# Kernel optimization log

Hardware: AMD Instinct MI355X
Metric: run time of the kernel (lower is better)

## Reference

```python
import jax, jax.numpy as jnp
import numpy as np

DIM = 2048
NUM_HEADS = 16
HEAD_DIM = DIM // NUM_HEADS
SCALE = 1.0 / float(np.sqrt(HEAD_DIM))


def setup_inputs() -> dict:
    key = jax.random.key(0)
    ks = jax.random.split(key, 7)
    B, L = 2, 2048
    x = jax.random.normal(ks[0], (B, L, DIM), dtype=jnp.float32)
    s = 1.0 / np.sqrt(DIM)
    # nn.Linear stores weight as [out, in]; y = x @ W.T + b
    Wq = jax.random.uniform(ks[1], (DIM, DIM), jnp.float32, -s, s)
    bq = jax.random.uniform(ks[2], (DIM,), jnp.float32, -s, s)
    Wk = jax.random.uniform(ks[3], (DIM, DIM), jnp.float32, -s, s)
    bk = jax.random.uniform(ks[4], (DIM,), jnp.float32, -s, s)
    Wv = jax.random.uniform(ks[5], (DIM, DIM), jnp.float32, -s, s)
    bv = jax.random.uniform(ks[6], (DIM,), jnp.float32, -s, s)
    return {"x": x, "Wq": Wq, "bq": bq, "Wk": Wk, "bk": bk, "Wv": Wv, "bv": bv}


def _attn(x, Wq, bq, Wk, bk, Wv, bv):
    B, L, D = x.shape
    H, Hd = NUM_HEADS, HEAD_DIM
    # projections: x @ W.T + b, then split heads -> [B, H, L, Hd]
    q = (x @ Wq.T + bq).reshape(B, L, H, Hd).transpose(0, 2, 1, 3)
    k = (x @ Wk.T + bk).reshape(B, L, H, Hd).transpose(0, 2, 1, 3)
    v = (x @ Wv.T + bv).reshape(B, L, H, Hd).transpose(0, 2, 1, 3)
    scores = jnp.einsum("bhqd,bhkd->bhqk", q, k) * SCALE  # [B,H,L,L]
    attn = jax.nn.softmax(scores, axis=-1)
    out = jnp.einsum("bhqk,bhkd->bhqd", attn, v)
    return out.transpose(0, 2, 1, 3).reshape(B, L, D)


def reference(x, Wq, bq, Wk, bk, Wv, bv):
    return _attn(x, Wq, bq, Wk, bk, Wv, bv)
```

## Files before the change

### kernel.cpp

```cpp
#include <hip/hip_runtime.h>
#include <stdint.h>

typedef unsigned short u16;
typedef __attribute__((ext_vector_type(8))) short short8;
typedef __attribute__((ext_vector_type(16))) float f32x16;

#define ATTN_SCALE 0.08838834764831845f

__device__ __forceinline__ u16 f2bf(float f) {
  union { float f; uint32_t u; } a; a.f = f;
  return (u16)((a.u + 0x7fffu + ((a.u >> 16) & 1u)) >> 16);
}

__device__ __forceinline__ void async16(const u16* g, u16* lds) {
  __builtin_amdgcn_global_load_lds(
      (const __attribute__((address_space(1))) void*)g,
      (__attribute__((address_space(3))) void*)lds, 16, 0, 0);
}

__global__ void cvt_kernel(const float* __restrict__ src, u16* __restrict__ dst, int n8) {
  int i = blockIdx.x * 256 + threadIdx.x;
  if (i >= n8) return;
  const float4* s4 = (const float4*)src;
  float4 a = s4[2 * i], c = s4[2 * i + 1];
  union { u16 h[8]; uint4 v; } o;
  o.h[0] = f2bf(a.x); o.h[1] = f2bf(a.y); o.h[2] = f2bf(a.z); o.h[3] = f2bf(a.w);
  o.h[4] = f2bf(c.x); o.h[5] = f2bf(c.y); o.h[6] = f2bf(c.z); o.h[7] = f2bf(c.w);
  ((uint4*)dst)[i] = o.v;
}

__global__ void cvtw_kernel(const float* __restrict__ w0, const float* __restrict__ w1,
                            const float* __restrict__ w2, u16* __restrict__ dst) {
  int z = blockIdx.y;
  const float* src = (z == 0) ? w0 : (z == 1) ? w1 : w2;
  int i = blockIdx.x * 256 + threadIdx.x;
  const float4* s4 = (const float4*)src;
  float4 a = s4[2 * i], c = s4[2 * i + 1];
  union { u16 h[8]; uint4 v; } o;
  o.h[0] = f2bf(a.x); o.h[1] = f2bf(a.y); o.h[2] = f2bf(a.z); o.h[3] = f2bf(a.w);
  o.h[4] = f2bf(c.x); o.h[5] = f2bf(c.y); o.h[6] = f2bf(c.z); o.h[7] = f2bf(c.w);
  ((uint4*)(dst + (size_t)z * 4194304))[i] = o.v;
}

__global__ __launch_bounds__(512, 2) void qkv_gemm(
    const u16* __restrict__ xb, const u16* __restrict__ Wb,
    const float* __restrict__ bq, const float* __restrict__ bk, const float* __restrict__ bv,
    u16* __restrict__ qkv) {
  extern __shared__ __align__(16) u16 smem[];
  u16* As = smem;
  u16* Bs = smem + 32768;
  const int z = blockIdx.z;
  const int n0 = blockIdx.x * 256, m0 = blockIdx.y * 256;
  const u16* Bw = Wb + (size_t)z * 4194304u;
  const float* bias = (z == 0) ? bq : (z == 1) ? bk : bv;
  u16* dst = qkv + (size_t)z * 8388608u;
  const int t = threadIdx.x;
  const int wave = t >> 6, lane = t & 63;
  const int wm = wave >> 2, wn = wave & 3, l31 = lane & 31, h = lane >> 5;

  int soff[2], goff[2];
#pragma unroll
  for (int p = 0; p < 2; ++p) {
    const int s = p * 512 + t;
    const int R = s >> 4, j = s & 15, u = j ^ (R & 15);
    const int m = 4 * R + (u >> 2), c = u & 3;
    soff[p] = s * 8;
    goff[p] = m * 2048 + c * 8;
  }
  const int q4 = (l31 & 3) * 4;
  int fr16A[4], fR15A[4], fr16B[2], fR15B[2];
#pragma unroll
  for (int am = 0; am < 4; ++am) {
    const int mA = wm * 128 + am * 32 + l31;
    fr16A[am] = (mA >> 2) * 16; fR15A[am] = (mA >> 2) & 15;
  }
#pragma unroll
  for (int bn = 0; bn < 2; ++bn) {
    const int mB = wn * 64 + bn * 32 + l31;
    fr16B[bn] = (mB >> 2) * 16; fR15B[bn] = (mB >> 2) & 15;
  }

  f32x16 acc[4][2];
#pragma unroll
  for (int am = 0; am < 4; ++am)
#pragma unroll
    for (int bn = 0; bn < 2; ++bn)
#pragma unroll
      for (int r = 0; r < 16; ++r) acc[am][bn][r] = 0.f;

  const u16* Abase = xb + (size_t)m0 * 2048;
  const u16* Bbase = Bw + (size_t)n0 * 2048;

#pragma unroll
  for (int r = 0; r < 3; ++r) {
    const int k0 = r * 32;
#pragma unroll
    for (int p = 0; p < 2; ++p) async16(Abase + goff[p] + k0, &As[r * 8192 + soff[p]]);
#pragma unroll
    for (int p = 0; p < 2; ++p) async16(Bbase + goff[p] + k0, &Bs[r * 8192 + soff[p]]);
  }

#pragma unroll 1
  for (int kt = 0; kt < 64; ++kt) {
    if (kt <= 61)      asm volatile("s_waitcnt vmcnt(8)" ::: "memory");
    else if (kt == 62) asm volatile("s_waitcnt vmcnt(4)" ::: "memory");
    else               asm volatile("s_waitcnt vmcnt(0)" ::: "memory");
    __builtin_amdgcn_s_barrier();
    __builtin_amdgcn_sched_barrier(0);

    if (kt + 3 < 64) {
      const int k0 = (kt + 3) * 32, bn_ = (kt + 3) & 3;
#pragma unroll
      for (int p = 0; p < 2; ++p) async16(Abase + goff[p] + k0, &As[bn_ * 8192 + soff[p]]);
#pragma unroll
      for (int p = 0; p < 2; ++p) async16(Bbase + goff[p] + k0, &Bs[bn_ * 8192 + soff[p]]);
    }

    const u16* aL = As + (kt & 3) * 8192;
    const u16* bL = Bs + (kt & 3) * 8192;
#pragma unroll
    for (int kk = 0; kk < 2; ++kk) {
      const int c = kk * 2 + h;
      short8 af[4], bf[2];
#pragma unroll
      for (int am = 0; am < 4; ++am)
        af[am] = *(const short8*)&aL[(fr16A[am] + ((q4 + c) ^ fR15A[am])) * 8];
#pragma unroll
      for (int bn = 0; bn < 2; ++bn)
        bf[bn] = *(const short8*)&bL[(fr16B[bn] + ((q4 + c) ^ fR15B[bn])) * 8];
      __builtin_amdgcn_s_setprio(1);
#pragma unroll
      for (int am = 0; am < 4; ++am)
#pragma unroll
        for (int bn = 0; bn < 2; ++bn)
          acc[am][bn] = __builtin_amdgcn_mfma_f32_32x32x16_bf16(af[am], bf[bn], acc[am][bn], 0, 0, 0);
      __builtin_amdgcn_s_setprio(0);
    }
  }

#pragma unroll
  for (int bn = 0; bn < 2; ++bn) {
    const int col = n0 + wn * 64 + bn * 32 + l31;
    const float bb_ = bias[col];
    const int hh = col >> 7, hd = col & 127;
#pragma unroll
    for (int am = 0; am < 4; ++am) {
#pragma unroll
      for (int g = 0; g < 4; ++g) {
        const int lbase = m0 + wm * 128 + am * 32 + 8 * g + 4 * h;
        const int bb = lbase >> 11, l0 = lbase & 2047;
        if (z == 2) {
          union { u16 q[4]; uint2 d; } pk;
#pragma unroll
          for (int rr = 0; rr < 4; ++rr) pk.q[rr] = f2bf(acc[am][bn][4 * g + rr] + bb_);
          *(uint2*)&dst[((size_t)(bb * 16 + hh) * 128 + hd) * 2048 + l0] = pk.d;
        } else {
#pragma unroll
          for (int rr = 0; rr < 4; ++rr)
            dst[((size_t)(bb * 16 + hh) * 2048 + (l0 + rr)) * 128 + hd] =
                f2bf(acc[am][bn][4 * g + rr] + bb_);
        }
      }
    }
  }
}

__global__ __launch_bounds__(256, 2) void attn_kernel(
    const u16* __restrict__ Qg,
    const u16* __restrict__ Kg,
    const u16* __restrict__ Vtg,
    float* __restrict__ out) {
  __shared__ __align__(16) u16 Ks[2][64 * 128];
  __shared__ __align__(16) u16 Vs[2][128 * 64];
  const int bh = blockIdx.y, q0 = blockIdx.x * 128;
  const int t = threadIdx.x, wave = t >> 6, lane = t & 63;
  const int l31 = lane & 31, h = lane >> 5;
  const u16* Qp = Qg + (size_t)bh * 262144;
  const u16* Kp = Kg + (size_t)bh * 262144;
  const u16* Vp = Vtg + (size_t)bh * 262144;
  const int b = bh >> 4, hd = bh & 15;
  const int qrow = q0 + wave * 32 + l31;

  short8 qf[8];
#pragma unroll
  for (int s = 0; s < 8; ++s)
    qf[s] = *(const short8*)&Qp[(size_t)qrow * 128 + s * 16 + h * 8];

  int kOff[4], kSlot[4], vOff[4], vSlot[4];
#pragma unroll
  for (int p = 0; p < 4; ++p) {
    const int s = p * 256 + wave * 64 + lane;
    const int rk = s >> 4, gk = (s & 15) ^ (rk & 15);
    kSlot[p] = s * 8; kOff[p] = rk * 128 + gk * 8;
    const int rv = s >> 3, gv = (s & 7) ^ (rv & 7);
    vSlot[p] = s * 8; vOff[p] = rv * 2048 + gv * 8;
  }

  f32x16 oac[4];
#pragma unroll
  for (int dt = 0; dt < 4; ++dt)
#pragma unroll
    for (int r = 0; r < 16; ++r) oac[dt][r] = 0.f;
  float den = 0.f;

#pragma unroll
  for (int p = 0; p < 4; ++p) async16(Kp + kOff[p], &Ks[0][kSlot[p]]);
#pragma unroll
  for (int p = 0; p < 4; ++p) async16(Vp + vOff[p], &Vs[0][vSlot[p]]);

#pragma unroll 1
  for (int kt = 0; kt < 32; ++kt) {
    __syncthreads();
    const int cur = kt & 1;
    if (kt + 1 < 32) {
      const int k1 = (kt + 1) * 64;
#pragma unroll
      for (int p = 0; p < 4; ++p)
        async16(Kp + (size_t)k1 * 128 + kOff[p], &Ks[cur ^ 1][kSlot[p]]);
#pragma unroll
      for (int p = 0; p < 4; ++p)
        async16(Vp + (size_t)k1 + vOff[p], &Vs[cur ^ 1][vSlot[p]]);
    }

#pragma unroll
    for (int T = 0; T < 2; ++T) {
      const int krow = T * 32 + l31;
      f32x16 sc;
#pragma unroll
      for (int r = 0; r < 16; ++r) sc[r] = 0.f;
#pragma unroll
      for (int s = 0; s < 8; ++s) {
        const short8 kf = *(const short8*)&Ks[cur][(krow * 16 + ((2 * s + h) ^ (krow & 15))) * 8];
        sc = __builtin_amdgcn_mfma_f32_32x32x16_bf16(kf, qf[s], sc, 0, 0, 0);
      }
      uint32_t pp[8];
#pragma unroll
      for (int i = 0; i < 8; ++i) {
        const float e0 = __expf(fminf(sc[2 * i] * ATTN_SCALE, 80.f));
        const float e1 = __expf(fminf(sc[2 * i + 1] * ATTN_SCALE, 80.f));
        den += e0 + e1;
        union { float f; uint32_t u; } u0, u1; u0.f = e0; u1.f = e1;
        pp[i] = ((u1.u + 0x8000u) & 0xffff0000u) | ((u0.u + 0x8000u) >> 16);
      }
      uint32_t x[8];
#pragma unroll
      for (int i = 0; i < 8; ++i) x[i] = __shfl_xor(pp[i], 32, 64);
#pragma unroll
      for (int ks = 0; ks < 2; ++ks) {
        const int o0 = ks * 4;
        union { uint32_t u[4]; short8 s8; } bfp;
        bfp.u[0] = h ? x[o0 + 2] : pp[o0 + 0];
        bfp.u[1] = h ? x[o0 + 3] : pp[o0 + 1];
        bfp.u[2] = h ? pp[o0 + 2] : x[o0 + 0];
        bfp.u[3] = h ? pp[o0 + 3] : x[o0 + 1];
        const int gk = T * 4 + ks * 2 + h;
#pragma unroll
        for (int dt = 0; dt < 4; ++dt) {
          const int vrow = dt * 32 + l31;
          const short8 vf = *(const short8*)&Vs[cur][(vrow * 8 + (gk ^ (vrow & 7))) * 8];
          oac[dt] = __builtin_amdgcn_mfma_f32_32x32x16_bf16(vf, bfp.s8, oac[dt], 0, 0, 0);
        }
      }
    }
  }

  den += __shfl_xor(den, 32, 64);
  const float inv = 1.f / den;
#pragma unroll
  for (int dt = 0; dt < 4; ++dt) {
#pragma unroll
    for (int g4 = 0; g4 < 4; ++g4) {
      float4 o;
      o.x = oac[dt][4 * g4 + 0] * inv;
      o.y = oac[dt][4 * g4 + 1] * inv;
      o.z = oac[dt][4 * g4 + 2] * inv;
      o.w = oac[dt][4 * g4 + 3] * inv;
      const int d = dt * 32 + g4 * 8 + h * 4;
      *(float4*)&out[((size_t)(b * 2048 + qrow)) * 2048 + hd * 128 + d] = o;
    }
  }
}

extern "C" void kernel_launch(void* const* d_in, const int* in_sizes, int n_in,
                              void* d_out, int out_size, void* d_ws, size_t ws_size,
                              hipStream_t stream) {
  const float* x  = (const float*)d_in[0];
  const float* Wq = (const float*)d_in[1];
  const float* bq = (const float*)d_in[2];
  const float* Wk = (const float*)d_in[3];
  const float* bk = (const float*)d_in[4];
  const float* Wv = (const float*)d_in[5];
  const float* bv = (const float*)d_in[6];
  float* out = (float*)d_out;
  if (ws_size < 92274688u) return;

  u16* xb  = (u16*)d_ws;
  u16* Wb  = xb + 8388608;
  u16* qkv = Wb + 12582912;

  cvt_kernel<<<4096, 256, 0, stream>>>(x, xb, 1048576);
  cvtw_kernel<<<dim3(2048, 3), 256, 0, stream>>>(Wq, Wk, Wv, Wb);
  qkv_gemm<<<dim3(8, 16, 3), 512, 131072, stream>>>(xb, Wb, bq, bk, bv, qkv);
  attn_kernel<<<dim3(16, 32), 256, 0, stream>>>(qkv, qkv + 8388608, qkv + 16777216, out);
}
```

Before: 355.3 us.

## Restructure projection GEMM mainloop into interleaved four-phase ping-pong schedule

Rewrites the K-loop of the QKV projection GEMM to process two 32-wide K chunks per iteration in four phases. Each phase interleaves LDS fragment reads, async global-to-LDS prefetch of either A or B for the next step, and the MFMA burst, with barriers and vmcnt waits placed between phases. Prefetch depth drops from three chunks ahead to a two-chunk lookahead. The aim is to spread memory issue across MFMA work and overlap loads with compute more evenly, at the cost of more barriers per K step and a shorter prefetch distance.

```diff
diff --git a/kernel.cpp b/kernel.cpp
--- a/kernel.cpp
+++ b/kernel.cpp
@@ -92,42 +92,46 @@
   const u16* Bbase = Bw + (size_t)n0 * 2048;
 
 #pragma unroll
-  for (int r = 0; r < 3; ++r) {
-    const int k0 = r * 32;
-#pragma unroll
-    for (int p = 0; p < 2; ++p) async16(Abase + goff[p] + k0, &As[r * 8192 + soff[p]]);
-#pragma unroll
-    for (int p = 0; p < 2; ++p) async16(Bbase + goff[p] + k0, &Bs[r * 8192 + soff[p]]);
-  }
+  for (int ch = 0; ch < 2; ++ch) {
+    const int k0 = ch * 32;
+#pragma unroll
+    for (int p = 0; p < 2; ++p) async16(Abase + goff[p] + k0, &As[ch * 8192 + soff[p]]);
+#pragma unroll
+    for (int p = 0; p < 2; ++p) async16(Bbase + goff[p] + k0, &Bs[ch * 8192 + soff[p]]);
+  }
+  asm volatile("s_waitcnt vmcnt(4)" ::: "memory");
+  __builtin_amdgcn_s_barrier();
 
 #pragma unroll 1
-  for (int kt = 0; kt < 64; ++kt) {
-    if (kt <= 61)      asm volatile("s_waitcnt vmcnt(8)" ::: "memory");
-    else if (kt == 62) asm volatile("s_waitcnt vmcnt(4)" ::: "memory");
-    else               asm volatile("s_waitcnt vmcnt(0)" ::: "memory");
-    __builtin_amdgcn_s_barrier();
-    __builtin_amdgcn_sched_barrier(0);
-
-    if (kt + 3 < 64) {
-      const int k0 = (kt + 3) * 32, bn_ = (kt + 3) & 3;
-#pragma unroll
-      for (int p = 0; p < 2; ++p) async16(Abase + goff[p] + k0, &As[bn_ * 8192 + soff[p]]);
-#pragma unroll
-      for (int p = 0; p < 2; ++p) async16(Bbase + goff[p] + k0, &Bs[bn_ * 8192 + soff[p]]);
-    }
-
-    const u16* aL = As + (kt & 3) * 8192;
-    const u16* bL = Bs + (kt & 3) * 8192;
-#pragma unroll
-    for (int kk = 0; kk < 2; ++kk) {
-      const int c = kk * 2 + h;
+  for (int kt = 0; kt < 32; ++kt) {
+    const int stage = (kt + 1 < 32);
+#pragma unroll
+    for (int ph = 0; ph < 4; ++ph) {
+      const int slot = ((2 * kt + (ph >> 1)) & 3) * 8192;
+      const int c = (ph & 1) * 2 + h;
       short8 af[4], bf[2];
 #pragma unroll
       for (int am = 0; am < 4; ++am)
-        af[am] = *(const short8*)&aL[(fr16A[am] + ((q4 + c) ^ fR15A[am])) * 8];
+        af[am] = *(const short8*)&As[slot + (fr16A[am] + ((q4 + c) ^ fR15A[am])) * 8];
 #pragma unroll
       for (int bn = 0; bn < 2; ++bn)
-        bf[bn] = *(const short8*)&bL[(fr16B[bn] + ((q4 + c) ^ fR15B[bn])) * 8];
+        bf[bn] = *(const short8*)&Bs[slot + (fr16B[bn] + ((q4 + c) ^ fR15B[bn])) * 8];
+
+      if (stage) {
+        const int ch = ph >> 1;
+        const int k0 = (kt + 1) * 64 + ch * 32;
+        const int ws = ((2 * kt + 2 + ch) & 3) * 8192;
+        if ((ph & 1) == 0) {
+#pragma unroll
+          for (int p = 0; p < 2; ++p) async16(Abase + goff[p] + k0, &As[ws + soff[p]]);
+        } else {
+#pragma unroll
+          for (int p = 0; p < 2; ++p) async16(Bbase + goff[p] + k0, &Bs[ws + soff[p]]);
+        }
+      }
+
+      __builtin_amdgcn_s_barrier();
+      asm volatile("s_waitcnt lgkmcnt(0)" ::: "memory");
       __builtin_amdgcn_s_setprio(1);
 #pragma unroll
       for (int am = 0; am < 4; ++am)
@@ -135,6 +139,14 @@
         for (int bn = 0; bn < 2; ++bn)
           acc[am][bn] = __builtin_amdgcn_mfma_f32_32x32x16_bf16(af[am], bf[bn], acc[am][bn], 0, 0, 0);
       __builtin_amdgcn_s_setprio(0);
+
+      if (ph == 1) {
+        if (stage) asm volatile("s_waitcnt vmcnt(4)" ::: "memory");
+        else       asm volatile("s_waitcnt vmcnt(0)" ::: "memory");
+      } else if (ph == 3) {
+        if (stage) asm volatile("s_waitcnt vmcnt(4)" ::: "memory");
+      }
+      __builtin_amdgcn_s_barrier();
     }
   }
 
```

New measurement: 356.4 us. About the same (+0.3%).

## Software-pipeline LDS fragment reads in QKV GEMM and remap attention block order

Applied to the files above, without the earlier changes.

Restructures the projection GEMM main loop so LDS fragment reads for the next half-step are issued before the MFMAs of the current half-step, with barriers between halves and global staging moved after the first MFMA batch. The aim is to hide LDS read latency behind matrix ops. It also remaps the attention kernel's block indices so consecutively scheduled blocks are spread across heads in a different order, which likely targets per-XCD cache locality. The cost is more live fragment registers and an extra barrier per iteration.

```diff
diff --git a/kernel.cpp b/kernel.cpp
--- a/kernel.cpp
+++ b/kernel.cpp
@@ -91,52 +91,53 @@
   const u16* Abase = xb + (size_t)m0 * 2048;
   const u16* Bbase = Bw + (size_t)n0 * 2048;
 
-#pragma unroll
-  for (int r = 0; r < 3; ++r) {
-    const int k0 = r * 32;
-#pragma unroll
-    for (int p = 0; p < 2; ++p) async16(Abase + goff[p] + k0, &As[r * 8192 + soff[p]]);
-#pragma unroll
-    for (int p = 0; p < 2; ++p) async16(Bbase + goff[p] + k0, &Bs[r * 8192 + soff[p]]);
-  }
+#define STAGE_CH(cc) { const int k0_ = (cc) * 32, ws_ = ((cc) & 3) * 8192;          \
+  _Pragma("unroll") for (int p = 0; p < 2; ++p)                                      \
+    async16(Abase + goff[p] + k0_, &As[ws_ + soff[p]]);                              \
+  _Pragma("unroll") for (int p = 0; p < 2; ++p)                                      \
+    async16(Bbase + goff[p] + k0_, &Bs[ws_ + soff[p]]); }
+
+#define RD_FRAGS(aa, bb, S_, cc_) {                                                  \
+  _Pragma("unroll") for (int am = 0; am < 4; ++am)                                   \
+    aa[am] = *(const short8*)&As[(S_) + (fr16A[am] + (((q4) + (cc_)) ^ fR15A[am])) * 8]; \
+  _Pragma("unroll") for (int bn = 0; bn < 2; ++bn)                                   \
+    bb[bn] = *(const short8*)&Bs[(S_) + (fr16B[bn] + (((q4) + (cc_)) ^ fR15B[bn])) * 8]; }
+
+#define DO_MFMA(aa, bb) {                                                            \
+  __builtin_amdgcn_s_setprio(1);                                                     \
+  _Pragma("unroll") for (int am = 0; am < 4; ++am)                                   \
+  _Pragma("unroll") for (int bn = 0; bn < 2; ++bn)                                   \
+    acc[am][bn] = __builtin_amdgcn_mfma_f32_32x32x16_bf16(aa[am], bb[bn], acc[am][bn], 0, 0, 0); \
+  __builtin_amdgcn_s_setprio(0); }
+
+  STAGE_CH(0); STAGE_CH(1); STAGE_CH(2);
+  asm volatile("s_waitcnt vmcnt(8)" ::: "memory");
+  __builtin_amdgcn_s_barrier();
+  __builtin_amdgcn_sched_barrier(0);
+
+  short8 ax[4], bx[2], ay[4], by[2];
+  RD_FRAGS(ax, bx, 0, h);
 
 #pragma unroll 1
-  for (int kt = 0; kt < 64; ++kt) {
-    if (kt <= 61)      asm volatile("s_waitcnt vmcnt(8)" ::: "memory");
-    else if (kt == 62) asm volatile("s_waitcnt vmcnt(4)" ::: "memory");
-    else               asm volatile("s_waitcnt vmcnt(0)" ::: "memory");
+  for (int c = 0; c < 64; ++c) {
+    const int S = (c & 3) * 8192;
+    RD_FRAGS(ay, by, S, 2 + h);
+    DO_MFMA(ax, bx);
+    if (c + 3 < 64) STAGE_CH(c + 3);
+    if (c <= 60)      asm volatile("s_waitcnt vmcnt(8)" ::: "memory");
+    else if (c == 61) asm volatile("s_waitcnt vmcnt(4)" ::: "memory");
+    else if (c == 62) asm volatile("s_waitcnt vmcnt(0)" ::: "memory");
     __builtin_amdgcn_s_barrier();
     __builtin_amdgcn_sched_barrier(0);
-
-    if (kt + 3 < 64) {
-      const int k0 = (kt + 3) * 32, bn_ = (kt + 3) & 3;
-#pragma unroll
-      for (int p = 0; p < 2; ++p) async16(Abase + goff[p] + k0, &As[bn_ * 8192 + soff[p]]);
-#pragma unroll
-      for (int p = 0; p < 2; ++p) async16(Bbase + goff[p] + k0, &Bs[bn_ * 8192 + soff[p]]);
-    }
-
-    const u16* aL = As + (kt & 3) * 8192;
-    const u16* bL = Bs + (kt & 3) * 8192;
-#pragma unroll
-    for (int kk = 0; kk < 2; ++kk) {
-      const int c = kk * 2 + h;
-      short8 af[4], bf[2];
-#pragma unroll
-      for (int am = 0; am < 4; ++am)
-        af[am] = *(const short8*)&aL[(fr16A[am] + ((q4 + c) ^ fR15A[am])) * 8];
-#pragma unroll
-      for (int bn = 0; bn < 2; ++bn)
-        bf[bn] = *(const short8*)&bL[(fr16B[bn] + ((q4 + c) ^ fR15B[bn])) * 8];
-      __builtin_amdgcn_s_setprio(1);
-#pragma unroll
-      for (int am = 0; am < 4; ++am)
-#pragma unroll
-        for (int bn = 0; bn < 2; ++bn)
-          acc[am][bn] = __builtin_amdgcn_mfma_f32_32x32x16_bf16(af[am], bf[bn], acc[am][bn], 0, 0, 0);
-      __builtin_amdgcn_s_setprio(0);
-    }
-  }
+    if (c + 1 < 64) { RD_FRAGS(ax, bx, ((c + 1) & 3) * 8192, h); }
+    DO_MFMA(ay, by);
+    __builtin_amdgcn_s_barrier();
+    __builtin_amdgcn_sched_barrier(0);
+  }
+
+#undef STAGE_CH
+#undef RD_FRAGS
+#undef DO_MFMA
 
 #pragma unroll
   for (int bn = 0; bn < 2; ++bn) {
@@ -172,7 +173,9 @@
     float* __restrict__ out) {
   __shared__ __align__(16) u16 Ks[2][64 * 128];
   __shared__ __align__(16) u16 Vs[2][128 * 64];
-  const int bh = blockIdx.y, q0 = blockIdx.x * 128;
+  const int s_lin = blockIdx.y * 16 + blockIdx.x;
+  const int w = (s_lin & 7) * 64 + (s_lin >> 3);
+  const int bh = w >> 4, q0 = (w & 15) * 128;
   const int t = threadIdx.x, wave = t >> 6, lane = t & 63;
   const int l31 = lane & 31, h = lane >> 5;
   const u16* Qp = Qg + (size_t)bh * 262144;
```

New measurement: 354.4 us. No clear change (-0.3%).

## Shrink QKV GEMM tile to 256x128 with double buffering; remap attention blocks

Applied to the files above, without the earlier changes.

The QKV projection GEMM moves from 512-thread 256x256 tiles with a 4-stage async LDS pipeline (128KB dynamic shared memory) to 256-thread 256x128 tiles with a 2-stage double buffer in static shared memory, doubling the grid. The aim is lower LDS use, higher occupancy and better CU fill. The cost is a shallower prefetch depth, with a full __syncthreads each iteration and less reuse of the B tile. The attention kernel also remaps block indices so that consecutive blocks are spread across heads and query tiles, presumably to balance L2 or XCD locality.

```diff
diff --git a/kernel.cpp b/kernel.cpp
--- a/kernel.cpp
+++ b/kernel.cpp
@@ -42,30 +42,37 @@
   ((uint4*)(dst + (size_t)z * 4194304))[i] = o.v;
 }
 
-__global__ __launch_bounds__(512, 2) void qkv_gemm(
+__global__ __launch_bounds__(256, 2) void qkv_gemm(
     const u16* __restrict__ xb, const u16* __restrict__ Wb,
     const float* __restrict__ bq, const float* __restrict__ bk, const float* __restrict__ bv,
     u16* __restrict__ qkv) {
-  extern __shared__ __align__(16) u16 smem[];
-  u16* As = smem;
-  u16* Bs = smem + 32768;
+  __shared__ __align__(16) u16 As[2][8192];
+  __shared__ __align__(16) u16 Bs[2][4096];
   const int z = blockIdx.z;
-  const int n0 = blockIdx.x * 256, m0 = blockIdx.y * 256;
+  const int n0 = blockIdx.x * 128, m0 = blockIdx.y * 256;
   const u16* Bw = Wb + (size_t)z * 4194304u;
   const float* bias = (z == 0) ? bq : (z == 1) ? bk : bv;
   u16* dst = qkv + (size_t)z * 8388608u;
   const int t = threadIdx.x;
   const int wave = t >> 6, lane = t & 63;
-  const int wm = wave >> 2, wn = wave & 3, l31 = lane & 31, h = lane >> 5;
-
-  int soff[2], goff[2];
-#pragma unroll
-  for (int p = 0; p < 2; ++p) {
-    const int s = p * 512 + t;
+  const int wm = wave >> 1, wn = wave & 1, l31 = lane & 31, h = lane >> 5;
+
+  int soffA[4], goffA[4], soffB[2], goffB[2];
+#pragma unroll
+  for (int p = 0; p < 4; ++p) {
+    const int s = p * 256 + t;
     const int R = s >> 4, j = s & 15, u = j ^ (R & 15);
     const int m = 4 * R + (u >> 2), c = u & 3;
-    soff[p] = s * 8;
-    goff[p] = m * 2048 + c * 8;
+    soffA[p] = s * 8;
+    goffA[p] = m * 2048 + c * 8;
+  }
+#pragma unroll
+  for (int p = 0; p < 2; ++p) {
+    const int s = p * 256 + t;
+    const int R = s >> 4, j = s & 15, u = j ^ (R & 15);
+    const int m = 4 * R + (u >> 2), c = u & 3;
+    soffB[p] = s * 8;
+    goffB[p] = m * 2048 + c * 8;
   }
   const int q4 = (l31 & 3) * 4;
   int fr16A[4], fR15A[4], fr16B[2], fR15B[2];
@@ -91,43 +98,33 @@
   const u16* Abase = xb + (size_t)m0 * 2048;
   const u16* Bbase = Bw + (size_t)n0 * 2048;
 
-#pragma unroll
-  for (int r = 0; r < 3; ++r) {
-    const int k0 = r * 32;
-#pragma unroll
-    for (int p = 0; p < 2; ++p) async16(Abase + goff[p] + k0, &As[r * 8192 + soff[p]]);
-#pragma unroll
-    for (int p = 0; p < 2; ++p) async16(Bbase + goff[p] + k0, &Bs[r * 8192 + soff[p]]);
-  }
-
 #pragma unroll 1
-  for (int kt = 0; kt < 64; ++kt) {
-    if (kt <= 61)      asm volatile("s_waitcnt vmcnt(8)" ::: "memory");
-    else if (kt == 62) asm volatile("s_waitcnt vmcnt(4)" ::: "memory");
-    else               asm volatile("s_waitcnt vmcnt(0)" ::: "memory");
-    __builtin_amdgcn_s_barrier();
-    __builtin_amdgcn_sched_barrier(0);
-
-    if (kt + 3 < 64) {
-      const int k0 = (kt + 3) * 32, bn_ = (kt + 3) & 3;
-#pragma unroll
-      for (int p = 0; p < 2; ++p) async16(Abase + goff[p] + k0, &As[bn_ * 8192 + soff[p]]);
-#pragma unroll
-      for (int p = 0; p < 2; ++p) async16(Bbase + goff[p] + k0, &Bs[bn_ * 8192 + soff[p]]);
-    }
-
-    const u16* aL = As + (kt & 3) * 8192;
-    const u16* bL = Bs + (kt & 3) * 8192;
-#pragma unroll
-    for (int kk = 0; kk < 2; ++kk) {
-      const int c = kk * 2 + h;
+  for (int n = 0; n < 64; ++n) {
+    if (n == 0) {
+#pragma unroll
+      for (int p = 0; p < 4; ++p) async16(Abase + goffA[p], &As[0][soffA[p]]);
+#pragma unroll
+      for (int p = 0; p < 2; ++p) async16(Bbase + goffB[p], &Bs[0][soffB[p]]);
+    }
+    __syncthreads();
+    const int cur = n & 1;
+    if (n + 1 < 64) {
+      const int k1 = (n + 1) * 32;
+#pragma unroll
+      for (int p = 0; p < 4; ++p) async16(Abase + goffA[p] + k1, &As[cur ^ 1][soffA[p]]);
+#pragma unroll
+      for (int p = 0; p < 2; ++p) async16(Bbase + goffB[p] + k1, &Bs[cur ^ 1][soffB[p]]);
+    }
+#pragma unroll
+    for (int ks = 0; ks < 2; ++ks) {
+      const int c = ks * 2 + h;
       short8 af[4], bf[2];
 #pragma unroll
       for (int am = 0; am < 4; ++am)
-        af[am] = *(const short8*)&aL[(fr16A[am] + ((q4 + c) ^ fR15A[am])) * 8];
+        af[am] = *(const short8*)&As[cur][(fr16A[am] + ((q4 + c) ^ fR15A[am])) * 8];
 #pragma unroll
       for (int bn = 0; bn < 2; ++bn)
-        bf[bn] = *(const short8*)&bL[(fr16B[bn] + ((q4 + c) ^ fR15B[bn])) * 8];
+        bf[bn] = *(const short8*)&Bs[cur][(fr16B[bn] + ((q4 + c) ^ fR15B[bn])) * 8];
       __builtin_amdgcn_s_setprio(1);
 #pragma unroll
       for (int am = 0; am < 4; ++am)
@@ -172,7 +169,9 @@
     float* __restrict__ out) {
   __shared__ __align__(16) u16 Ks[2][64 * 128];
   __shared__ __align__(16) u16 Vs[2][128 * 64];
-  const int bh = blockIdx.y, q0 = blockIdx.x * 128;
+  const int s_lin = blockIdx.y * 16 + blockIdx.x;
+  const int w = (s_lin & 7) * 64 + (s_lin >> 3);
+  const int bh = w >> 4, q0 = (w & 15) * 128;
   const int t = threadIdx.x, wave = t >> 6, lane = t & 63;
   const int l31 = lane & 31, h = lane >> 5;
   const u16* Qp = Qg + (size_t)bh * 262144;
@@ -300,6 +299,6 @@
 
   cvt_kernel<<<4096, 256, 0, stream>>>(x, xb, 1048576);
   cvtw_kernel<<<dim3(2048, 3), 256, 0, stream>>>(Wq, Wk, Wv, Wb);
-  qkv_gemm<<<dim3(8, 16, 3), 512, 131072, stream>>>(xb, Wb, bq, bk, bv, qkv);
+  qkv_gemm<<<dim3(16, 16, 3), 256, 0, stream>>>(xb, Wb, bq, bk, bv, qkv);
   attn_kernel<<<dim3(16, 32), 256, 0, stream>>>(qkv, qkv + 8388608, qkv + 16777216, out);
 }
```

Measured after the change: 369.2 us. 3.9% more time.
